# Kernel tuning notes

Measured on AMD Instinct MI355X. Metric: run time of the kernel, lower is better.

Reference implementation:

```python
import jax, jax.numpy as jnp
import numpy as np

B, T, E, A = 512, 64, 1024, 32
S, D, H = 30, 200, 200          # stoch, deter, hidden
SS = D + S                      # state_size = 230
MIN_STD = 0.1
UPDATE_BIAS = -1.0
W_SCALE = 0.05


def setup_inputs() -> dict:
    key = jax.random.key(0)
    ks = jax.random.split(key, 17)
    n = jax.random.normal
    return {
        "embed":       n(ks[0], (B, T, E), jnp.float32),
        "action":      n(ks[1], (B, T, A), jnp.float32),
        "context":     n(ks[2], (B, T, SS), jnp.float32),
        "noise_prior": n(ks[3], (T, B, S), jnp.float32),
        "noise_post":  n(ks[4], (T, B, S), jnp.float32),
        "w_inp":       n(ks[5], (S + SS + A, H), jnp.float32) * W_SCALE,
        "b_inp":       jnp.zeros((H,), jnp.float32),
        "w_gru":       n(ks[6], (H + D, 3 * D), jnp.float32) * W_SCALE,
        "b_gru":       jnp.zeros((3 * D,), jnp.float32),
        "w_img_out":   n(ks[7], (D, H), jnp.float32) * W_SCALE,
        "b_img_out":   jnp.zeros((H,), jnp.float32),
        "w_obs_out":   n(ks[8], (D + E, H), jnp.float32) * W_SCALE,
        "b_obs_out":   jnp.zeros((H,), jnp.float32),
        "w_ims_stat":  n(ks[9], (H, 2 * S), jnp.float32) * W_SCALE,
        "b_ims_stat":  jnp.zeros((2 * S,), jnp.float32),
        "w_obs_stat":  n(ks[10], (H, 2 * S), jnp.float32) * W_SCALE,
        "b_obs_stat":  jnp.zeros((2 * S,), jnp.float32),
    }


def _observe(embed, action, context, noise_prior, noise_post,
             w_inp, b_inp, w_gru, b_gru, w_img_out, b_img_out,
             w_obs_out, b_obs_out, w_ims_stat, b_ims_stat,
             w_obs_stat, b_obs_stat):
    # time-major
    emb_t = jnp.swapaxes(embed, 0, 1)    # [T,B,E]
    act_t = jnp.swapaxes(action, 0, 1)   # [T,B,A]
    ctx_t = jnp.swapaxes(context, 0, 1)  # [T,B,SS]

    def step(carry, xs):
        stoch, deter = carry
        ctx, act, emb, n_p, n_o = xs
        # img_step: input MLP + GRU cell
        x = jnp.concatenate([stoch, ctx, act], -1)
        x = jax.nn.elu(x @ w_inp + b_inp)
        parts = jnp.concatenate([x, deter], -1) @ w_gru + b_gru
        reset, cand, update = jnp.split(parts, 3, -1)
        reset = jax.nn.sigmoid(reset)
        cand = jnp.tanh(reset * cand)
        update = jax.nn.sigmoid(update + UPDATE_BIAS)
        deter_new = update * cand + (1.0 - update) * deter
        # prior stats
        h = jax.nn.elu(deter_new @ w_img_out + b_img_out)
        st = h @ w_ims_stat + b_ims_stat
        pm, ps = jnp.split(st, 2, -1)
        ps = jax.nn.softplus(ps) + MIN_STD
        p_stoch = pm + ps * n_p
        # posterior stats
        ho = jax.nn.elu(jnp.concatenate([deter_new, emb], -1) @ w_obs_out + b_obs_out)
        so = ho @ w_obs_stat + b_obs_stat
        om, os_ = jnp.split(so, 2, -1)
        os_ = jax.nn.softplus(os_) + MIN_STD
        o_stoch = om + os_ * n_o
        out = jnp.concatenate([om, os_, o_stoch, pm, ps, p_stoch, deter_new], -1)
        return (o_stoch, deter_new), out

    carry0 = (jnp.zeros((B, S), embed.dtype), jnp.zeros((B, D), embed.dtype))
    _, ys = jax.lax.scan(step, carry0, (ctx_t, act_t, emb_t, noise_prior, noise_post))
    # ys: [T,B,6S+D] -> [B,T,6S+D]  (post mean/std/stoch, prior mean/std/stoch, deter)
    return jnp.swapaxes(ys, 0, 1)


def reference(embed, action, context, noise_prior, noise_post,
              w_inp, b_inp, w_gru, b_gru, w_img_out, b_img_out,
              w_obs_out, b_obs_out, w_ims_stat, b_ims_stat,
              w_obs_stat, b_obs_stat):
    return _observe(embed, action, context, noise_prior, noise_post,
                    w_inp, b_inp, w_gru, b_gru, w_img_out, b_img_out,
                    w_obs_out, b_obs_out, w_ims_stat, b_ims_stat,
                    w_obs_stat, b_obs_stat)
```

## Files before the change

kernel.cpp:

```cpp
#include <hip/hip_runtime.h>
#include <cstddef>

typedef short short8 __attribute__((ext_vector_type(8)));
typedef float f32x4 __attribute__((ext_vector_type(4)));
typedef unsigned short u16;

#define Bn 512
#define Tn 64
#define En 1024
#define An 32
#define Sn 30
#define Dn 200
#define SSn 230
#define OUTC 380

#define U16_WINP0  0
#define U16_WINPCA 6656
#define U16_WGRU   66560
#define U16_WIMG   326144
#define U16_WOBSD  372736
#define U16_WIMS   419328
#define U16_WOBSS  433664
#define U16_WOBSE  448000
#define U16_PREO   660992
#define U16_PREI   7214592

#define WINP0_8  0
#define WINPCA_8 832
#define WGRU_8   8320
#define WIMG_8   40768
#define WOBSD_8  46592
#define WIMS_8   52416
#define WOBSS_8  54208
#define WOBSE_8  56000

#define DEV static __device__ __forceinline__
#define MFMA(a,b,c) __builtin_amdgcn_mfma_f32_16x16x32_bf16((a),(b),(c),0,0,0)

DEV u16 f2bf(float f) {
  union { float f; unsigned u; } v; v.f = f;
  return (u16)((v.u + 0x7FFFu + ((v.u >> 16) & 1u)) >> 16);
}
DEV float bf2f(u16 h) {
  union { unsigned u; float f; } v; v.u = ((unsigned)h) << 16; return v.f;
}
DEV float fexp(float x)  { return __builtin_amdgcn_exp2f(x * 1.44269504f); }
DEV float sigm(float x)  { return __builtin_amdgcn_rcpf(1.f + fexp(-x)); }
DEV float tanhf_(float x){ return 1.f - 2.f * __builtin_amdgcn_rcpf(fexp(2.f * x) + 1.f); }
DEV float elu1(float x)  { return x > 0.f ? x : fexp(x) - 1.f; }
DEV float splus(float x) { return 0.69314718f * __builtin_amdgcn_logf(1.f + fexp(x)); }

__global__ __launch_bounds__(256) void k_pack2(
    const float* __restrict__ w_inp, const float* __restrict__ w_gru,
    const float* __restrict__ w_img, const float* __restrict__ w_obs,
    const float* __restrict__ w_ims, const float* __restrict__ w_obss,
    u16* __restrict__ ws) {
  int s = blockIdx.x;
  const float* src; int KT, Kr, ldN, roff, colbase, cmax; size_t dstbase; int ntKT;
  if (s < 13)      { src=w_inp;  KT=1;  Kr=30;   ldN=200; roff=0;   int nt=s;    colbase=nt*16; cmax=min(16,200-colbase); dstbase=U16_WINP0;  ntKT=nt*KT; }
  else if (s < 26) { src=w_inp;  KT=9;  Kr=262;  ldN=200; roff=30;  int nt=s-13; colbase=nt*16; cmax=min(16,200-colbase); dstbase=U16_WINPCA; ntKT=nt*KT; }
  else if (s < 65) { src=w_gru;  KT=13; Kr=400;  ldN=600; roff=0;   int ntp=s-26; int g=ntp/3, p=ntp%3;
                     colbase=p*200+g*16; cmax=min(16,200-g*16); dstbase=U16_WGRU; ntKT=ntp*KT; }
  else if (s < 78) { src=w_img;  KT=7;  Kr=200;  ldN=200; roff=0;   int nt=s-65; colbase=nt*16; cmax=min(16,200-colbase); dstbase=U16_WIMG;  ntKT=nt*KT; }
  else if (s < 91) { src=w_obs;  KT=7;  Kr=200;  ldN=200; roff=0;   int nt=s-78; colbase=nt*16; cmax=min(16,200-colbase); dstbase=U16_WOBSD; ntKT=nt*KT; }
  else if (s < 95) { src=w_ims;  KT=7;  Kr=200;  ldN=60;  roff=0;   int nt=s-91; colbase=nt*16; cmax=min(16,60-colbase);  dstbase=U16_WIMS;  ntKT=nt*KT; }
  else if (s < 99) { src=w_obss; KT=7;  Kr=200;  ldN=60;  roff=0;   int nt=s-95; colbase=nt*16; cmax=min(16,60-colbase);  dstbase=U16_WOBSS; ntKT=nt*KT; }
  else             { src=w_obs;  KT=32; Kr=1024; ldN=200; roff=200; int nt=s-99; colbase=nt*16; cmax=min(16,200-colbase); dstbase=U16_WOBSE; ntKT=nt*KT; }

  __shared__ float Ws[2048];
  int tid = threadIdx.x;
  int nchunk = (KT + 3) >> 2;
  for (int kc = 0; kc < nchunk; ++kc) {
    __syncthreads();
    for (int i = tid; i < 2048; i += 256) {
      int r = i >> 4, c = i & 15;
      int k = kc * 128 + r;
      Ws[i] = (k < Kr && c < cmax) ? src[(size_t)(roff + k) * ldN + colbase + c] : 0.f;
    }
    __syncthreads();
    int nf = KT - kc * 4; if (nf > 4) nf = 4;
    int fi = tid >> 6, lane = tid & 63;
    if (fi < nf) {
      int kt = kc * 4 + fi;
      union { u16 h[8]; short8 v; } pk;
#pragma unroll
      for (int j = 0; j < 8; ++j)
        pk.h[j] = f2bf(Ws[(fi * 32 + ((lane >> 4) << 3) + j) * 16 + (lane & 15)]);
      *(short8*)&ws[dstbase + (size_t)(ntKT + kt) * 512 + lane * 8] = pk.v;
    }
  }
}

__global__ __launch_bounds__(256) void k_pre(
    const float* __restrict__ emb, const float* __restrict__ ctx,
    const float* __restrict__ act, const float* __restrict__ b_obs,
    const float* __restrict__ b_inp, u16* __restrict__ ws) {
  __shared__ u16 Asm[64 * 72];
  __shared__ short8 Bsm[26 * 64];
  const short8* Wb = (const short8*)ws;
  u16* preO = ws + U16_PREO;
  u16* preI = ws + U16_PREI;

  int tid = threadIdx.x, wv = tid >> 6, lane = tid & 63;
  int lrow = lane & 15, quad = lane >> 4;
  int m0 = blockIdx.x * 64;
  int t = m0 >> 9, b0 = m0 & 511;

  const f32x4 z4 = {0.f, 0.f, 0.f, 0.f};
  f32x4 acc[13];

#pragma unroll
  for (int i = 0; i < 13; ++i) acc[i] = z4;
  for (int kc = 0; kc < 16; ++kc) {
    __syncthreads();
#pragma unroll
    for (int q = 0; q < 4; ++q) {
      int i = tid + q * 256;
      int row = i >> 4, c4 = i & 15;
      const float* src = emb + ((size_t)((b0 + row) * Tn + t)) * En + kc * 64 + c4 * 4;
      float4 v = *(const float4*)src;
      union { u16 h[4]; unsigned long long ll; } p;
      p.h[0] = f2bf(v.x); p.h[1] = f2bf(v.y); p.h[2] = f2bf(v.z); p.h[3] = f2bf(v.w);
      *(unsigned long long*)&Asm[row * 72 + c4 * 4] = p.ll;
    }
    for (int q = 0; q < 7; ++q) {
      int i = tid + q * 256;
      if (i < 1664) {
        int pair = i >> 6, l = i & 63;
        int ktl = pair / 13, nt = pair % 13;
        Bsm[i] = Wb[WOBSE_8 + (size_t)(nt * 32 + kc * 2 + ktl) * 64 + l];
      }
    }
    __syncthreads();
#pragma unroll
    for (int ktl = 0; ktl < 2; ++ktl) {
      short8 a = *(const short8*)&Asm[(wv * 16 + lrow) * 72 + ktl * 32 + quad * 8];
#pragma unroll
      for (int nt = 0; nt < 13; ++nt)
        acc[nt] = MFMA(a, Bsm[(ktl * 13 + nt) * 64 + lane], acc[nt]);
    }
  }
#pragma unroll
  for (int nt = 0; nt < 13; ++nt) {
    int col = nt * 16 + lrow;
    if (col < 200) {
      float bias = b_obs[col];
#pragma unroll
      for (int r = 0; r < 4; ++r) {
        int m = t * 512 + b0 + wv * 16 + quad * 4 + r;
        preO[(size_t)m * 200 + col] = f2bf(acc[nt][r] + bias);
      }
    }
  }

#pragma unroll
  for (int i = 0; i < 13; ++i) acc[i] = z4;
  for (int kc = 0; kc < 5; ++kc) {
    __syncthreads();
#pragma unroll
    for (int q = 0; q < 4; ++q) {
      int i = tid + q * 256;
      int row = i >> 4, c4 = i & 15;
      union { u16 h[4]; unsigned long long ll; } p;
#pragma unroll
      for (int e = 0; e < 4; ++e) {
        int k = kc * 64 + c4 * 4 + e;
        float v = 0.f;
        if (k < 230)      v = ctx[((size_t)(b0 + row) * Tn + t) * SSn + k];
        else if (k < 262) v = act[((size_t)(b0 + row) * Tn + t) * An + (k - 230)];
        p.h[e] = f2bf(v);
      }
      *(unsigned long long*)&Asm[row * 72 + c4 * 4] = p.ll;
    }
    int nktl = (kc < 4) ? 2 : 1;
    for (int q = 0; q < 7; ++q) {
      int i = tid + q * 256;
      if (i < nktl * 13 * 64) {
        int pair = i >> 6, l = i & 63;
        int ktl = pair / 13, nt = pair % 13;
        Bsm[i] = Wb[WINPCA_8 + (size_t)(nt * 9 + kc * 2 + ktl) * 64 + l];
      }
    }
    __syncthreads();
    for (int ktl = 0; ktl < nktl; ++ktl) {
      short8 a = *(const short8*)&Asm[(wv * 16 + lrow) * 72 + ktl * 32 + quad * 8];
#pragma unroll
      for (int nt = 0; nt < 13; ++nt)
        acc[nt] = MFMA(a, Bsm[(ktl * 13 + nt) * 64 + lane], acc[nt]);
    }
  }
#pragma unroll
  for (int nt = 0; nt < 13; ++nt) {
    int col = nt * 16 + lrow;
    if (col < 200) {
      float bias = b_inp[col];
#pragma unroll
      for (int r = 0; r < 4; ++r) {
        int m = t * 512 + b0 + wv * 16 + quad * 4 + r;
        preI[(size_t)m * 200 + col] = f2bf(acc[nt][r] + bias);
      }
    }
  }
}

__global__ __launch_bounds__(512, 2) void k_scan(
    const float* __restrict__ g_no, const float* __restrict__ b_gru,
    const float* __restrict__ b_obss, const u16* __restrict__ ws,
    float* __restrict__ out) {

  __shared__ u16 AB[16 * 872];
  __shared__ u16 Uin[16 * 40];
  __shared__ u16 hoA[16 * 232];
  __shared__ float sto[16 * 66];

  const short8* Wb = (const short8*)ws;
  const u16* preO = ws + U16_PREO;
  const u16* preI = ws + U16_PREI;

  const int tid = threadIdx.x, wv = tid >> 6, lane = tid & 63;
  const int lrow = lane & 15, quad = lane >> 4;
  const int b0 = blockIdx.x * 16;
  const f32x4 z4 = {0.f, 0.f, 0.f, 0.f};

  const bool two = wv < 5;
  const int colA0 = wv * 16 + lrow;
  const int colA1 = (wv + 8) * 16 + lrow;
  const int dcol0 = colA0;
  const int dcol1 = colA1;
  const int nrow = tid / 30, ns = tid - nrow * 30;

  short8 fA0 = Wb[WINP0_8 + (size_t)wv * 64 + lane];
  short8 fA1 = two ? Wb[WINP0_8 + (size_t)(wv + 8) * 64 + lane] : fA0;

  float bgr0 = b_gru[dcol0], bgc0 = b_gru[200 + dcol0], bgu0 = b_gru[400 + dcol0];
  float bgr1 = 0.f, bgc1 = 0.f, bgu1 = 0.f;
  if (two && dcol1 < 200) { bgr1 = b_gru[dcol1]; bgc1 = b_gru[200 + dcol1]; bgu1 = b_gru[400 + dcol1]; }
  const int cD = (wv & 3) * 16 + lrow;
  const float bD = (wv < 4 && cD < 60) ? b_obss[cD] : 0.f;

  for (int i = tid; i < 16 * 872; i += 512) AB[i] = 0;
  for (int i = tid; i < 16 * 40; i += 512) Uin[i] = 0;
  for (int i = tid; i < 16 * 232; i += 512) hoA[i] = 0;
  __syncthreads();

  for (int t = 0; t < Tn; ++t) {
    const int par = t & 1;
    const int pb = par * 424, qb = 424 - pb;

    u16 pin0[4], pin1[4] = {0,0,0,0}, pob0[4], pob1[4] = {0,0,0,0};
    {
      size_t mb = (size_t)t * 512 + b0 + quad * 4;
#pragma unroll
      for (int r = 0; r < 4; ++r) pin0[r] = preI[(mb + r) * 200 + colA0];
      if (two && colA1 < 200) {
#pragma unroll
        for (int r = 0; r < 4; ++r) pin1[r] = preI[(mb + r) * 200 + colA1];
      }
#pragma unroll
      for (int r = 0; r < 4; ++r) pob0[r] = preO[(mb + r) * 200 + colA0];
      if (two && colA1 < 200) {
#pragma unroll
        for (int r = 0; r < 4; ++r) pob1[r] = preO[(mb + r) * 200 + colA1];
      }
    }
    float vno = 0.f;
    if (tid < 480) vno = g_no[((size_t)t * 512 + b0 + nrow) * Sn + ns];

    __syncthreads();

    {
      short8 aU = *(const short8*)&Uin[lrow * 40 + quad * 8];
      f32x4 a0 = MFMA(aU, fA0, z4);
#pragma unroll
      for (int r = 0; r < 4; ++r)
        AB[(quad * 4 + r) * 872 + pb + colA0] = f2bf(elu1(a0[r] + bf2f(pin0[r])));
      if (two) {
        f32x4 a1 = MFMA(aU, fA1, z4);
        if (colA1 < 200) {
#pragma unroll
          for (int r = 0; r < 4; ++r)
            AB[(quad * 4 + r) * 872 + pb + colA1] = f2bf(elu1(a1[r] + bf2f(pin1[r])));
        }
      }
    }
    __syncthreads();

    {
      short8 ax[13];
#pragma unroll
      for (int kt = 0; kt < 13; ++kt)
        ax[kt] = *(const short8*)&AB[lrow * 872 + pb + kt * 32 + quad * 8];
      const int ng = two ? 2 : 1;
      for (int gi = 0; gi < ng; ++gi) {
        int g = wv + 8 * gi;
        int dcol = gi ? dcol1 : dcol0;
        float br = gi ? bgr1 : bgr0, bc = gi ? bgc1 : bgc0, bu = gi ? bgu1 : bgu0;
        const short8* bpr = Wb + WGRU_8 + (size_t)((3 * g + 0) * 13) * 64 + lane;
        const short8* bpc = Wb + WGRU_8 + (size_t)((3 * g + 1) * 13) * 64 + lane;
        const short8* bpu = Wb + WGRU_8 + (size_t)((3 * g + 2) * 13) * 64 + lane;
        f32x4 ar = z4, ac = z4, au = z4;
#pragma unroll
        for (int kt = 0; kt < 13; ++kt) ar = MFMA(ax[kt], bpr[kt * 64], ar);
#pragma unroll
        for (int kt = 0; kt < 13; ++kt) ac = MFMA(ax[kt], bpc[kt * 64], ac);
#pragma unroll
        for (int kt = 0; kt < 13; ++kt) au = MFMA(ax[kt], bpu[kt * 64], au);
        if (dcol < 200) {
#pragma unroll
          for (int r = 0; r < 4; ++r) {
            int row = quad * 4 + r;
            float dold = bf2f(AB[row * 872 + pb + 200 + dcol]);
            float rs = sigm(ar[r] + br);
            float cnd = tanhf_(rs * (ac[r] + bc));
            float up = sigm(au[r] + bu - 1.f);
            float dn = up * cnd + (1.f - up) * dold;
            AB[row * 872 + qb + 200 + dcol] = f2bf(dn);
            __builtin_nontemporal_store(dn, &out[((size_t)(b0 + row) * Tn + t) * OUTC + 180 + dcol]);
          }
        }
      }
    }
    __syncthreads();

    {
      short8 ad[7];
#pragma unroll
      for (int kt = 0; kt < 7; ++kt)
        ad[kt] = *(const short8*)&AB[lrow * 872 + qb + 200 + kt * 32 + quad * 8];
      {
        const short8* bp = Wb + WOBSD_8 + (size_t)(wv * 7) * 64 + lane;
        f32x4 a0 = z4;
#pragma unroll
        for (int kt = 0; kt < 7; ++kt) a0 = MFMA(ad[kt], bp[kt * 64], a0);
#pragma unroll
        for (int r = 0; r < 4; ++r)
          hoA[(quad * 4 + r) * 232 + colA0] = f2bf(elu1(a0[r] + bf2f(pob0[r])));
      }
      if (two && colA1 < 200) {
        const short8* bp = Wb + WOBSD_8 + (size_t)((wv + 8) * 7) * 64 + lane;
        f32x4 a1 = z4;
#pragma unroll
        for (int kt = 0; kt < 7; ++kt) a1 = MFMA(ad[kt], bp[kt * 64], a1);
#pragma unroll
        for (int r = 0; r < 4; ++r)
          hoA[(quad * 4 + r) * 232 + colA1] = f2bf(elu1(a1[r] + bf2f(pob1[r])));
      }
    }
    __syncthreads();

    if (wv < 4) {
      const short8* bp = Wb + WOBSS_8 + (size_t)(wv * 7) * 64 + lane;
      f32x4 acc = z4;
#pragma unroll
      for (int kt = 0; kt < 7; ++kt) {
        short8 a = *(const short8*)&hoA[lrow * 232 + kt * 32 + quad * 8];
        acc = MFMA(a, bp[kt * 64], acc);
      }
      if (cD < 60) {
#pragma unroll
        for (int r = 0; r < 4; ++r) sto[(quad * 4 + r) * 66 + cD] = acc[r] + bD;
      }
    }
    __syncthreads();

    if (tid < 480) {
      size_t ob = ((size_t)(b0 + nrow) * Tn + t) * OUTC;
      float om = sto[nrow * 66 + ns];
      float os = splus(sto[nrow * 66 + 30 + ns]) + 0.1f;
      float ost = om + os * vno;
      __builtin_nontemporal_store(om,  &out[ob + ns]);
      __builtin_nontemporal_store(os,  &out[ob + 30 + ns]);
      __builtin_nontemporal_store(ost, &out[ob + 60 + ns]);
      Uin[nrow * 40 + ns] = f2bf(ost);
    }
  }
}

__global__ __launch_bounds__(256) void k_prior(
    const float* __restrict__ g_np, const float* __restrict__ b_img,
    const float* __restrict__ b_ims, const u16* __restrict__ ws,
    float* __restrict__ out) {
  __shared__ u16 Ad[64 * 232];
  __shared__ u16 Ah[64 * 232];
  __shared__ float stf[64 * 66];
  const short8* Wb = (const short8*)ws;

  int tid = threadIdx.x, wv = tid >> 6, lane = tid & 63;
  int lrow = lane & 15, quad = lane >> 4;
  int b = blockIdx.x;
  const f32x4 z4 = {0.f, 0.f, 0.f, 0.f};

  for (int i = tid; i < 64 * 232; i += 256) { Ad[i] = 0; Ah[i] = 0; }
  __syncthreads();

  for (int idx = tid; idx < 64 * 200; idx += 256) {
    int row = idx / 200, col = idx - row * 200;
    Ad[row * 232 + col] = f2bf(out[((size_t)b * Tn + row) * OUTC + 180 + col]);
  }
  __syncthreads();

  {
    short8 af[7];
#pragma unroll
    for (int kt = 0; kt < 7; ++kt)
      af[kt] = *(const short8*)&Ad[(wv * 16 + lrow) * 232 + kt * 32 + quad * 8];
    for (int nt = 0; nt < 13; ++nt) {
      const short8* bp = Wb + WIMG_8 + (size_t)(nt * 7) * 64 + lane;
      f32x4 acc = z4;
#pragma unroll
      for (int kt = 0; kt < 7; ++kt) acc = MFMA(af[kt], bp[kt * 64], acc);
      int col = nt * 16 + lrow;
      if (col < 200) {
        float bias = b_img[col];
#pragma unroll
        for (int r = 0; r < 4; ++r)
          Ah[(wv * 16 + quad * 4 + r) * 232 + col] = f2bf(elu1(acc[r] + bias));
      }
    }
  }
  __syncthreads();

  {
    short8 ah[7];
#pragma unroll
    for (int kt = 0; kt < 7; ++kt)
      ah[kt] = *(const short8*)&Ah[(wv * 16 + lrow) * 232 + kt * 32 + quad * 8];
#pragma unroll
    for (int nt = 0; nt < 4; ++nt) {
      const short8* bp = Wb + WIMS_8 + (size_t)(nt * 7) * 64 + lane;
      f32x4 acc = z4;
#pragma unroll
      for (int kt = 0; kt < 7; ++kt) acc = MFMA(ah[kt], bp[kt * 64], acc);
      int col = nt * 16 + lrow;
      if (col < 60) {
        float bias = b_ims[col];
#pragma unroll
        for (int r = 0; r < 4; ++r)
          stf[(wv * 16 + quad * 4 + r) * 66 + col] = acc[r] + bias;
      }
    }
  }
  __syncthreads();

  for (int idx = tid; idx < 64 * 30; idx += 256) {
    int row = idx / 30, s = idx - row * 30;
    float pm = stf[row * 66 + s];
    float ps = splus(stf[row * 66 + 30 + s]) + 0.1f;
    float pst = pm + ps * g_np[((size_t)row * 512 + b) * Sn + s];
    size_t ob = ((size_t)b * Tn + row) * OUTC;
    __builtin_nontemporal_store(pm,  &out[ob + 90 + s]);
    __builtin_nontemporal_store(ps,  &out[ob + 120 + s]);
    __builtin_nontemporal_store(pst, &out[ob + 150 + s]);
  }
}

extern "C" void kernel_launch(void* const* d_in, const int* in_sizes, int n_in,
                              void* d_out, int out_size, void* d_ws, size_t ws_size,
                              hipStream_t stream) {
  (void)in_sizes; (void)n_in; (void)out_size; (void)ws_size;
  const float* emb    = (const float*)d_in[0];
  const float* action = (const float*)d_in[1];
  const float* ctx    = (const float*)d_in[2];
  const float* np_    = (const float*)d_in[3];
  const float* no_    = (const float*)d_in[4];
  const float* w_inp  = (const float*)d_in[5];
  const float* b_inp  = (const float*)d_in[6];
  const float* w_gru  = (const float*)d_in[7];
  const float* b_gru  = (const float*)d_in[8];
  const float* w_img  = (const float*)d_in[9];
  const float* b_img  = (const float*)d_in[10];
  const float* w_obs  = (const float*)d_in[11];
  const float* b_obs  = (const float*)d_in[12];
  const float* w_ims  = (const float*)d_in[13];
  const float* b_ims  = (const float*)d_in[14];
  const float* w_obss = (const float*)d_in[15];
  const float* b_obss = (const float*)d_in[16];

  u16* wsu = (u16*)d_ws;
  float* out = (float*)d_out;

  k_pack2<<<112, 256, 0, stream>>>(w_inp, w_gru, w_img, w_obs, w_ims, w_obss, wsu);
  k_pre<<<512, 256, 0, stream>>>(emb, ctx, action, b_obs, b_inp, wsu);
  k_scan<<<32, 512, 0, stream>>>(no_, b_gru, b_obss, wsu, out);
  k_prior<<<512, 256, 0, stream>>>(np_, b_img, b_ims, wsu, out);
}
```

Baseline: 1.226 ms.

## Prefetch next-step inputs, hoist first weight tiles, interleave GRU MFMAs, use LDS-only barriers

The scan kernel now loads the next timestep's preI/preO/noise values during the current step, removing the global-load latency from the start of each step. It also keeps the first k-tile of each weight slice in registers across steps and interleaves the two column groups' GRU MFMA chains for more independent work. It folds the update bias into the bias constant and replaces __syncthreads with a barrier that waits only on LDS counters, so in-flight global loads and stores do not stall each barrier. Launch bounds drop from 2 to 1 blocks per CU to give more register room, which risks lower occupancy.

```diff
diff --git a/kernel.cpp b/kernel.cpp
--- a/kernel.cpp
+++ b/kernel.cpp
@@ -49,6 +49,12 @@
 DEV float tanhf_(float x){ return 1.f - 2.f * __builtin_amdgcn_rcpf(fexp(2.f * x) + 1.f); }
 DEV float elu1(float x)  { return x > 0.f ? x : fexp(x) - 1.f; }
 DEV float splus(float x) { return 0.69314718f * __builtin_amdgcn_logf(1.f + fexp(x)); }
+
+DEV void barx() {
+  asm volatile("s_waitcnt lgkmcnt(0)" ::: "memory");
+  __builtin_amdgcn_s_barrier();
+  asm volatile("" ::: "memory");
+}
 
 __global__ __launch_bounds__(256) void k_pack2(
     const float* __restrict__ w_inp, const float* __restrict__ w_gru,
@@ -203,7 +209,7 @@
   }
 }
 
-__global__ __launch_bounds__(512, 2) void k_scan(
+__global__ __launch_bounds__(512, 1) void k_scan(
     const float* __restrict__ g_no, const float* __restrict__ b_gru,
     const float* __restrict__ b_obss, const u16* __restrict__ ws,
     float* __restrict__ out) {
@@ -223,156 +229,226 @@
   const f32x4 z4 = {0.f, 0.f, 0.f, 0.f};
 
   const bool two = wv < 5;
+  const int g1 = two ? (wv + 8) : wv;
   const int colA0 = wv * 16 + lrow;
-  const int colA1 = (wv + 8) * 16 + lrow;
+  const int colA1 = g1 * 16 + lrow;
   const int dcol0 = colA0;
   const int dcol1 = colA1;
   const int nrow = tid / 30, ns = tid - nrow * 30;
 
   short8 fA0 = Wb[WINP0_8 + (size_t)wv * 64 + lane];
-  short8 fA1 = two ? Wb[WINP0_8 + (size_t)(wv + 8) * 64 + lane] : fA0;
-
-  float bgr0 = b_gru[dcol0], bgc0 = b_gru[200 + dcol0], bgu0 = b_gru[400 + dcol0];
-  float bgr1 = 0.f, bgc1 = 0.f, bgu1 = 0.f;
-  if (two && dcol1 < 200) { bgr1 = b_gru[dcol1]; bgc1 = b_gru[200 + dcol1]; bgu1 = b_gru[400 + dcol1]; }
+  short8 fA1 = Wb[WINP0_8 + (size_t)g1 * 64 + lane];
+
+  float bgr0 = b_gru[dcol0], bgc0 = b_gru[200 + dcol0], bgu0 = b_gru[400 + dcol0] - 1.f;
+  float bgr1 = 0.f, bgc1 = 0.f, bgu1 = -1.f;
+  if (two && dcol1 < 200) { bgr1 = b_gru[dcol1]; bgc1 = b_gru[200 + dcol1]; bgu1 = b_gru[400 + dcol1] - 1.f; }
   const int cD = (wv & 3) * 16 + lrow;
   const float bD = (wv < 4 && cD < 60) ? b_obss[cD] : 0.f;
+
+  const short8* pr0 = Wb + WGRU_8 + (size_t)((3 * wv + 0) * 13) * 64 + lane;
+  const short8* pc0 = Wb + WGRU_8 + (size_t)((3 * wv + 1) * 13) * 64 + lane;
+  const short8* pu0 = Wb + WGRU_8 + (size_t)((3 * wv + 2) * 13) * 64 + lane;
+  const short8* pr1 = Wb + WGRU_8 + (size_t)((3 * g1 + 0) * 13) * 64 + lane;
+  const short8* pc1 = Wb + WGRU_8 + (size_t)((3 * g1 + 1) * 13) * 64 + lane;
+  const short8* pu1 = Wb + WGRU_8 + (size_t)((3 * g1 + 2) * 13) * 64 + lane;
+  const short8* c0p = Wb + WOBSD_8 + (size_t)(wv * 7) * 64 + lane;
+  const short8* c1p = Wb + WOBSD_8 + (size_t)(g1 * 7) * 64 + lane;
+  const short8* bpD = Wb + WOBSS_8 + (size_t)(((wv < 4) ? wv : 0) * 7) * 64 + lane;
+
+  const short8 wBr0 = pr0[0], wBc0 = pc0[0], wBu0 = pu0[0];
+  const short8 wBr1 = pr1[0], wBc1 = pc1[0], wBu1 = pu1[0];
+  const short8 wC0 = c0p[0], wC1 = c1p[0];
+  const short8 wD0 = bpD[0];
 
   for (int i = tid; i < 16 * 872; i += 512) AB[i] = 0;
   for (int i = tid; i < 16 * 40; i += 512) Uin[i] = 0;
   for (int i = tid; i < 16 * 232; i += 512) hoA[i] = 0;
   __syncthreads();
 
+  u16 pinC0[4], pinC1[4] = {0,0,0,0}, pobC0[4], pobC1[4] = {0,0,0,0};
+  float vnoC = 0.f;
+  {
+    size_t mb = (size_t)b0 + quad * 4;
+#pragma unroll
+    for (int r = 0; r < 4; ++r) pinC0[r] = preI[(mb + r) * 200 + colA0];
+#pragma unroll
+    for (int r = 0; r < 4; ++r) pobC0[r] = preO[(mb + r) * 200 + colA0];
+    if (two && colA1 < 200) {
+#pragma unroll
+      for (int r = 0; r < 4; ++r) pinC1[r] = preI[(mb + r) * 200 + colA1];
+#pragma unroll
+      for (int r = 0; r < 4; ++r) pobC1[r] = preO[(mb + r) * 200 + colA1];
+    }
+    if (tid < 480) vnoC = g_no[((size_t)b0 + nrow) * Sn + ns];
+  }
+
   for (int t = 0; t < Tn; ++t) {
     const int par = t & 1;
     const int pb = par * 424, qb = 424 - pb;
 
-    u16 pin0[4], pin1[4] = {0,0,0,0}, pob0[4], pob1[4] = {0,0,0,0};
-    {
-      size_t mb = (size_t)t * 512 + b0 + quad * 4;
-#pragma unroll
-      for (int r = 0; r < 4; ++r) pin0[r] = preI[(mb + r) * 200 + colA0];
-      if (two && colA1 < 200) {
-#pragma unroll
-        for (int r = 0; r < 4; ++r) pin1[r] = preI[(mb + r) * 200 + colA1];
-      }
-#pragma unroll
-      for (int r = 0; r < 4; ++r) pob0[r] = preO[(mb + r) * 200 + colA0];
-      if (two && colA1 < 200) {
-#pragma unroll
-        for (int r = 0; r < 4; ++r) pob1[r] = preO[(mb + r) * 200 + colA1];
-      }
-    }
-    float vno = 0.f;
-    if (tid < 480) vno = g_no[((size_t)t * 512 + b0 + nrow) * Sn + ns];
-
-    __syncthreads();
+    barx();
 
     {
       short8 aU = *(const short8*)&Uin[lrow * 40 + quad * 8];
       f32x4 a0 = MFMA(aU, fA0, z4);
 #pragma unroll
       for (int r = 0; r < 4; ++r)
-        AB[(quad * 4 + r) * 872 + pb + colA0] = f2bf(elu1(a0[r] + bf2f(pin0[r])));
+        AB[(quad * 4 + r) * 872 + pb + colA0] = f2bf(elu1(a0[r] + bf2f(pinC0[r])));
       if (two) {
         f32x4 a1 = MFMA(aU, fA1, z4);
         if (colA1 < 200) {
 #pragma unroll
           for (int r = 0; r < 4; ++r)
-            AB[(quad * 4 + r) * 872 + pb + colA1] = f2bf(elu1(a1[r] + bf2f(pin1[r])));
+            AB[(quad * 4 + r) * 872 + pb + colA1] = f2bf(elu1(a1[r] + bf2f(pinC1[r])));
         }
       }
     }
-    __syncthreads();
+
+    u16 pinN0[4], pinN1[4] = {0,0,0,0}, pobN0[4], pobN1[4] = {0,0,0,0};
+    float vnoN = 0.f;
+    {
+      int tn = (t + 1 < Tn) ? (t + 1) : t;
+      size_t mb = (size_t)tn * 512 + b0 + quad * 4;
+#pragma unroll
+      for (int r = 0; r < 4; ++r) pinN0[r] = preI[(mb + r) * 200 + colA0];
+#pragma unroll
+      for (int r = 0; r < 4; ++r) pobN0[r] = preO[(mb + r) * 200 + colA0];
+      if (two && colA1 < 200) {
+#pragma unroll
+        for (int r = 0; r < 4; ++r) pinN1[r] = preI[(mb + r) * 200 + colA1];
+#pragma unroll
+        for (int r = 0; r < 4; ++r) pobN1[r] = preO[(mb + r) * 200 + colA1];
+      }
+      if (tid < 480) vnoN = g_no[((size_t)tn * 512 + b0 + nrow) * Sn + ns];
+    }
+
+    barx();
 
     {
       short8 ax[13];
 #pragma unroll
       for (int kt = 0; kt < 13; ++kt)
         ax[kt] = *(const short8*)&AB[lrow * 872 + pb + kt * 32 + quad * 8];
-      const int ng = two ? 2 : 1;
-      for (int gi = 0; gi < ng; ++gi) {
-        int g = wv + 8 * gi;
-        int dcol = gi ? dcol1 : dcol0;
-        float br = gi ? bgr1 : bgr0, bc = gi ? bgc1 : bgc0, bu = gi ? bgu1 : bgu0;
-        const short8* bpr = Wb + WGRU_8 + (size_t)((3 * g + 0) * 13) * 64 + lane;
-        const short8* bpc = Wb + WGRU_8 + (size_t)((3 * g + 1) * 13) * 64 + lane;
-        const short8* bpu = Wb + WGRU_8 + (size_t)((3 * g + 2) * 13) * 64 + lane;
-        f32x4 ar = z4, ac = z4, au = z4;
-#pragma unroll
-        for (int kt = 0; kt < 13; ++kt) ar = MFMA(ax[kt], bpr[kt * 64], ar);
-#pragma unroll
-        for (int kt = 0; kt < 13; ++kt) ac = MFMA(ax[kt], bpc[kt * 64], ac);
-#pragma unroll
-        for (int kt = 0; kt < 13; ++kt) au = MFMA(ax[kt], bpu[kt * 64], au);
-        if (dcol < 200) {
-#pragma unroll
-          for (int r = 0; r < 4; ++r) {
-            int row = quad * 4 + r;
-            float dold = bf2f(AB[row * 872 + pb + 200 + dcol]);
-            float rs = sigm(ar[r] + br);
-            float cnd = tanhf_(rs * (ac[r] + bc));
-            float up = sigm(au[r] + bu - 1.f);
-            float dn = up * cnd + (1.f - up) * dold;
-            AB[row * 872 + qb + 200 + dcol] = f2bf(dn);
-            __builtin_nontemporal_store(dn, &out[((size_t)(b0 + row) * Tn + t) * OUTC + 180 + dcol]);
-          }
+      f32x4 ar0, ac0, au0, ar1 = z4, ac1 = z4, au1 = z4;
+      ar0 = MFMA(ax[0], wBr0, z4);
+      ac0 = MFMA(ax[0], wBc0, z4);
+      au0 = MFMA(ax[0], wBu0, z4);
+      if (two) {
+        ar1 = MFMA(ax[0], wBr1, z4);
+        ac1 = MFMA(ax[0], wBc1, z4);
+        au1 = MFMA(ax[0], wBu1, z4);
+#pragma unroll
+        for (int kt = 1; kt < 13; ++kt) {
+          ar0 = MFMA(ax[kt], pr0[kt * 64], ar0);
+          ar1 = MFMA(ax[kt], pr1[kt * 64], ar1);
+          ac0 = MFMA(ax[kt], pc0[kt * 64], ac0);
+          ac1 = MFMA(ax[kt], pc1[kt * 64], ac1);
+          au0 = MFMA(ax[kt], pu0[kt * 64], au0);
+          au1 = MFMA(ax[kt], pu1[kt * 64], au1);
         }
-      }
-    }
-    __syncthreads();
+      } else {
+#pragma unroll
+        for (int kt = 1; kt < 13; ++kt) {
+          ar0 = MFMA(ax[kt], pr0[kt * 64], ar0);
+          ac0 = MFMA(ax[kt], pc0[kt * 64], ac0);
+          au0 = MFMA(ax[kt], pu0[kt * 64], au0);
+        }
+      }
+#pragma unroll
+      for (int r = 0; r < 4; ++r) {
+        int row = quad * 4 + r;
+        float dold = bf2f(AB[row * 872 + pb + 200 + dcol0]);
+        float rs = sigm(ar0[r] + bgr0);
+        float cnd = tanhf_(rs * (ac0[r] + bgc0));
+        float up = sigm(au0[r] + bgu0);
+        float dn = up * cnd + (1.f - up) * dold;
+        AB[row * 872 + qb + 200 + dcol0] = f2bf(dn);
+        __builtin_nontemporal_store(dn, &out[((size_t)(b0 + row) * Tn + t) * OUTC + 180 + dcol0]);
+      }
+      if (two && dcol1 < 200) {
+#pragma unroll
+        for (int r = 0; r < 4; ++r) {
+          int row = quad * 4 + r;
+          float dold = bf2f(AB[row * 872 + pb + 200 + dcol1]);
+          float rs = sigm(ar1[r] + bgr1);
+          float cnd = tanhf_(rs * (ac1[r] + bgc1));
+          float up = sigm(au1[r] + bgu1);
+          float dn = up * cnd + (1.f - up) * dold;
+          AB[row * 872 + qb + 200 + dcol1] = f2bf(dn);
+          __builtin_nontemporal_store(dn, &out[((size_t)(b0 + row) * Tn + t) * OUTC + 180 + dcol1]);
+        }
+      }
+    }
+
+    barx();
 
     {
       short8 ad[7];
 #pragma unroll
       for (int kt = 0; kt < 7; ++kt)
         ad[kt] = *(const short8*)&AB[lrow * 872 + qb + 200 + kt * 32 + quad * 8];
+      f32x4 h0, h1 = z4;
+      h0 = MFMA(ad[0], wC0, z4);
+      if (two) {
+        h1 = MFMA(ad[0], wC1, z4);
+#pragma unroll
+        for (int kt = 1; kt < 7; ++kt) {
+          h0 = MFMA(ad[kt], c0p[kt * 64], h0);
+          h1 = MFMA(ad[kt], c1p[kt * 64], h1);
+        }
+      } else {
+#pragma unroll
+        for (int kt = 1; kt < 7; ++kt)
+          h0 = MFMA(ad[kt], c0p[kt * 64], h0);
+      }
+#pragma unroll
+      for (int r = 0; r < 4; ++r)
+        hoA[(quad * 4 + r) * 232 + colA0] = f2bf(elu1(h0[r] + bf2f(pobC0[r])));
+      if (two && colA1 < 200) {
+#pragma unroll
+        for (int r = 0; r < 4; ++r)
+          hoA[(quad * 4 + r) * 232 + colA1] = f2bf(elu1(h1[r] + bf2f(pobC1[r])));
+      }
+    }
+
+    barx();
+
+    if (wv < 4) {
+      f32x4 acc;
       {
-        const short8* bp = Wb + WOBSD_8 + (size_t)(wv * 7) * 64 + lane;
-        f32x4 a0 = z4;
-#pragma unroll
-        for (int kt = 0; kt < 7; ++kt) a0 = MFMA(ad[kt], bp[kt * 64], a0);
-#pragma unroll
-        for (int r = 0; r < 4; ++r)
-          hoA[(quad * 4 + r) * 232 + colA0] = f2bf(elu1(a0[r] + bf2f(pob0[r])));
-      }
-      if (two && colA1 < 200) {
-        const short8* bp = Wb + WOBSD_8 + (size_t)((wv + 8) * 7) * 64 + lane;
-        f32x4 a1 = z4;
-#pragma unroll
-        for (int kt = 0; kt < 7; ++kt) a1 = MFMA(ad[kt], bp[kt * 64], a1);
-#pragma unroll
-        for (int r = 0; r < 4; ++r)
-          hoA[(quad * 4 + r) * 232 + colA1] = f2bf(elu1(a1[r] + bf2f(pob1[r])));
-      }
-    }
-    __syncthreads();
-
-    if (wv < 4) {
-      const short8* bp = Wb + WOBSS_8 + (size_t)(wv * 7) * 64 + lane;
-      f32x4 acc = z4;
-#pragma unroll
-      for (int kt = 0; kt < 7; ++kt) {
+        short8 a = *(const short8*)&hoA[lrow * 232 + quad * 8];
+        acc = MFMA(a, wD0, z4);
+      }
+#pragma unroll
+      for (int kt = 1; kt < 7; ++kt) {
         short8 a = *(const short8*)&hoA[lrow * 232 + kt * 32 + quad * 8];
-        acc = MFMA(a, bp[kt * 64], acc);
+        acc = MFMA(a, bpD[kt * 64], acc);
       }
       if (cD < 60) {
 #pragma unroll
         for (int r = 0; r < 4; ++r) sto[(quad * 4 + r) * 66 + cD] = acc[r] + bD;
       }
     }
-    __syncthreads();
+
+    barx();
 
     if (tid < 480) {
       size_t ob = ((size_t)(b0 + nrow) * Tn + t) * OUTC;
       float om = sto[nrow * 66 + ns];
       float os = splus(sto[nrow * 66 + 30 + ns]) + 0.1f;
-      float ost = om + os * vno;
+      float ost = om + os * vnoC;
       __builtin_nontemporal_store(om,  &out[ob + ns]);
       __builtin_nontemporal_store(os,  &out[ob + 30 + ns]);
       __builtin_nontemporal_store(ost, &out[ob + 60 + ns]);
       Uin[nrow * 40 + ns] = f2bf(ost);
     }
+
+#pragma unroll
+    for (int r = 0; r < 4; ++r) {
+      pinC0[r] = pinN0[r]; pinC1[r] = pinN1[r];
+      pobC0[r] = pobN0[r]; pobC1[r] = pobN1[r];
+    }
+    vnoC = vnoN;
   }
 }
 
```

Result: slower. 1.335 ms (+8.9%).
